# Optimization experiments

Hardware: AMD Instinct MI355X
Metric: run time of the kernel (lower is better)

## Reference

```python
import jax, jax.numpy as jnp
import numpy as np

DIM = 768
HEADS = 12
DIM_HEAD = DIM // HEADS
FACTOR = DIM_HEAD ** (-0.5)
B, T = 4, 2048


def setup_inputs() -> dict:
    key = jax.random.key(0)
    k1, k2, k3 = jax.random.split(key, 3)
    x = jax.random.normal(k1, (B, T, DIM), dtype=jnp.float32)
    # VarianceScaling-like init scale for linear weights
    W_qkv = jax.random.normal(k2, (DIM, 3 * DIM), dtype=jnp.float32) * (DIM ** -0.5)
    W_out = jax.random.normal(k3, (DIM, DIM), dtype=jnp.float32) * (DIM ** -0.5)
    return {"x": x, "W_qkv": W_qkv, "W_out": W_out}


def reference(x, W_qkv, W_out):
    b, t, _ = x.shape
    qkv = x @ W_qkv  # [b, t, 3*dim]
    # einops 'b t (d k h) -> k b h t d' with k=3, h=HEADS: d slowest, k middle, h fastest
    qkv = qkv.reshape(b, t, DIM_HEAD, 3, HEADS)
    qkv = jnp.transpose(qkv, (3, 0, 4, 1, 2))  # [3, b, h, t, d]
    q, k, v = qkv[0], qkv[1], qkv[2]
    # scaled dot-product attention, full [b,h,t,t] scores as in the original
    scores = jnp.einsum('bhid,bhjd->bhij', q, k) * FACTOR
    attn = jax.nn.softmax(scores, axis=-1)
    out = jnp.einsum('bhij,bhjd->bhid', attn, v)  # [b, h, t, d]
    # 'b h t d -> b t (h d)'
    out = jnp.transpose(out, (0, 2, 1, 3)).reshape(b, t, HEADS * DIM_HEAD)
    return out @ W_out
```

## Files before the change

kernel.cpp:

```cpp
#include <hip/hip_runtime.h>
#include <hip/hip_bf16.h>

#define DIM    768
#define HEADS  12
#define DHEAD  64
#define BATCH  4
#define SEQ    2048
#define NROW   (BATCH * SEQ)
#define QKVN   (3 * DIM)
#define FACTOR 0.125f
#define QSCALE 0.18033688011112042f

typedef __attribute__((ext_vector_type(8))) short short8;
typedef __attribute__((ext_vector_type(4))) float floatx4;

__device__ __forceinline__ floatx4 mfma16(short8 a, short8 b, floatx4 c) {
    return __builtin_amdgcn_mfma_f32_16x16x32_bf16(a, b, c, 0, 0, 0);
}

__device__ __forceinline__ void glds16(const void* g, void* l) {
    __builtin_amdgcn_global_load_lds((const __attribute__((address_space(1))) void*)g,
                                     (__attribute__((address_space(3))) void*)l,
                                     16, 0, 0);
}

__device__ __forceinline__ short rne16(float f) {
    unsigned u = __builtin_bit_cast(unsigned, f);
    return (short)((u + 0x7fffu + ((u >> 16) & 1u)) >> 16);
}
__device__ __forceinline__ unsigned pack2(float lo, float hi) {
    unsigned ul = __builtin_bit_cast(unsigned, lo);
    unsigned uh = __builtin_bit_cast(unsigned, hi);
    ul = (ul + 0x7fffu + ((ul >> 16) & 1u)) >> 16;
    uh = (uh + 0x7fffu + ((uh >> 16) & 1u)) & 0xffff0000u;
    return ul | uh;
}
__device__ __forceinline__ unsigned cvtpk(float lo, float hi) {
    unsigned r;
    asm("v_cvt_pk_bf16_f32 %0, %1, %2" : "=v"(r) : "v"(lo), "v"(hi));
    return r;
}

__device__ __forceinline__ int swz8(int row, int col) {
    return (row << 6) + ((((col >> 3) ^ row) & 7) << 3) + (col & 7);
}

__global__ __launch_bounds__(256) void prep(const float* __restrict__ x,
                                            short* __restrict__ xb,
                                            const float* __restrict__ Wqkv,
                                            short* __restrict__ Wqt,
                                            const float* __restrict__ Wout,
                                            short* __restrict__ Wot) {
    __shared__ short T[32][33];
    int blk = blockIdx.x;
    if (blk < 6144) {
        int g = blk * 256 + threadIdx.x;
        float4 v = ((const float4*)x)[g];
        uint2 o;
        o.x = pack2(v.x, v.y);
        o.y = pack2(v.z, v.w);
        ((uint2*)xb)[g] = o;
        return;
    }
    blk -= 6144;
    const float* W;
    short* Wt;
    int N, permute, bx, by;
    if (blk < 1728) { W = Wqkv; Wt = Wqt; N = QKVN; permute = 1; bx = blk % 72; by = blk / 72; }
    else { blk -= 1728; W = Wout; Wt = Wot; N = DIM; permute = 0; bx = blk % 24; by = blk / 24; }

    int n0 = bx * 32, k0 = by * 32;
    int c = threadIdx.x & 31, r0 = threadIdx.x >> 5;
    for (int r = r0; r < 32; r += 8)
        T[r][c] = rne16(W[(size_t)(k0 + r) * N + n0 + c]);
    __syncthreads();
    for (int r = r0; r < 32; r += 8) {
        int n = n0 + r;
        int np = n;
        float scale = 1.0f;
        if (permute) {
            int d = n / 36, rem = n - d * 36;
            int which = rem / 12, h = rem - which * 12;
            np = which * 768 + h * 64 + d;
            if (which == 0) scale = QSCALE;
        }
        float v = __bfloat162float(__hip_bfloat16_raw{(unsigned short)T[c][r]});
        Wt[(size_t)np * DIM + k0 + c] = (scale == 1.0f) ? T[c][r] : rne16(v * scale);
    }
}

__global__ __launch_bounds__(256) void gemm_qkv(const short* __restrict__ A,
                                                const short* __restrict__ Bt,
                                                short* __restrict__ Qo,
                                                short* __restrict__ Ko,
                                                short* __restrict__ Vto) {
    __shared__ short As[128 * 64];
    __shared__ short Bs[128 * 64];
    const int tid = threadIdx.x;
    const int lane = tid & 63, wave = tid >> 6;
    const int l15 = lane & 15, quad = lane >> 4;

    const int flat = blockIdx.x;
    const int xcd = flat & 7;
    const int local = flat >> 3;
    const int mloc = local & 7, nloc = local >> 3;
    const int m0 = (xcd * 8 + mloc) * 128;
    const int n0 = nloc * 128;

    const int wm = (wave >> 1) * 64, wn = (wave & 1) * 64;
    const int r8 = wave * 8 + (lane >> 3);
    const int c8 = lane & 7;
    const int sc = ((c8 ^ (r8 & 7)) << 3);

    const int sn = n0 + wn;
    const int which = sn / 768;
    const bool swapAB = (which != 2);

    floatx4 acc[4][4] = {};
    for (int k0 = 0; k0 < DIM; k0 += 64) {
#pragma unroll
        for (int i = 0; i < 4; ++i) {
            int row = i * 32 + r8;
            glds16(&A[(size_t)(m0 + row) * DIM + k0 + sc], &As[(size_t)(i * 32 + wave * 8) * 64]);
            glds16(&Bt[(size_t)(n0 + row) * DIM + k0 + sc], &Bs[(size_t)(i * 32 + wave * 8) * 64]);
        }
        __syncthreads();
#pragma unroll
        for (int ks = 0; ks < 2; ++ks) {
            short8 a[4], b[4];
#pragma unroll
            for (int mt = 0; mt < 4; ++mt)
                a[mt] = *(const short8*)&As[swz8(wm + mt * 16 + l15, ks * 32 + quad * 8)];
#pragma unroll
            for (int nt = 0; nt < 4; ++nt)
                b[nt] = *(const short8*)&Bs[swz8(wn + nt * 16 + l15, ks * 32 + quad * 8)];
            if (swapAB) {
#pragma unroll
                for (int mt = 0; mt < 4; ++mt)
#pragma unroll
                    for (int nt = 0; nt < 4; ++nt)
                        acc[mt][nt] = mfma16(b[nt], a[mt], acc[mt][nt]);
            } else {
#pragma unroll
                for (int mt = 0; mt < 4; ++mt)
#pragma unroll
                    for (int nt = 0; nt < 4; ++nt)
                        acc[mt][nt] = mfma16(a[mt], b[nt], acc[mt][nt]);
            }
        }
        __syncthreads();
    }

    const int h = (sn - which * 768) >> 6;
    const int bb = (m0 + wm) >> 11;
    const int tbase = (m0 + wm) & 2047;
    const size_t tilebase = ((size_t)(bb * HEADS + h) * 32 + (tbase >> 6)) * 4096;

    if (which != 2) {
        short* dst = (which == 0) ? Qo : Ko;
#pragma unroll
        for (int mt = 0; mt < 4; ++mt)
#pragma unroll
            for (int nt = 0; nt < 4; ++nt) {
                int tl = mt * 16 + l15;
                int d0 = nt * 16 + quad * 4;
                uint2 pk;
                pk.x = pack2(acc[mt][nt][0], acc[mt][nt][1]);
                pk.y = pack2(acc[mt][nt][2], acc[mt][nt][3]);
                *(uint2*)&dst[tilebase + swz8(tl, d0)] = pk;
            }
    } else {
        short* vld = ((wave < 2) ? As : Bs) + (wave & 1) * 4096;
#pragma unroll
        for (int mt = 0; mt < 4; ++mt)
#pragma unroll
            for (int nt = 0; nt < 4; ++nt) {
                int d = nt * 16 + l15;
                int tl = mt * 16 + quad * 4;
                int chunk = (tl >> 3) ^ (d & 7);
                int addr = (d << 6) + (chunk << 3) + (tl & 7);
                uint2 pk;
                pk.x = pack2(acc[mt][nt][0], acc[mt][nt][1]);
                pk.y = pack2(acc[mt][nt][2], acc[mt][nt][3]);
                *(uint2*)&vld[addr] = pk;
            }
    }
    __syncthreads();
    if (which == 2) {
        short* vld = ((wave < 2) ? As : Bs) + (wave & 1) * 4096;
#pragma unroll
        for (int i = 0; i < 8; ++i) {
            int c = (i * 64 + lane) * 8;
            *(uint4*)&Vto[tilebase + c] = *(const uint4*)&vld[c];
        }
    }
}

__global__ __launch_bounds__(256, 3) void attn_mfma(const short* __restrict__ Q,
                                                    const short* __restrict__ K,
                                                    const short* __restrict__ Vt,
                                                    short* __restrict__ O) {
    __shared__ __align__(16) short smem[24576];
    const int tid = threadIdx.x;
    const int lane = tid & 63, wave = tid >> 6;
    const int l15 = lane & 15, quad = lane >> 4;
    const int flat = blockIdx.x;
    const int xcd = flat & 7, li = flat >> 3;
    const int bh = xcd + (li % 6) * 8;
    const int q0 = (li / 6) * 128;
    const size_t base = (size_t)bh * SEQ * DHEAD;
    short* Pp = smem + 16384 + wave * 2048;
    const int lane8 = lane * 8;

    {
        size_t qtb = base + (size_t)(q0 >> 6) * 4096;
#pragma unroll
        for (int c = 0; c < 4; ++c) {
            int i = wave * 4 + c;
            glds16(&Q[qtb + (size_t)i * 512 + lane8], &smem[i * 512]);
        }
    }
    __syncthreads();
    short8 qf[2][2];
#pragma unroll
    for (int mt = 0; mt < 2; ++mt)
#pragma unroll
        for (int ks = 0; ks < 2; ++ks)
            qf[mt][ks] = *(const short8*)&smem[(wave >> 1) * 4096 +
                                               swz8((wave & 1) * 32 + mt * 16 + l15,
                                                    ks * 32 + quad * 8)];
    __syncthreads();

    floatx4 o[4][2] = {};
    float lsum[2] = {0.f, 0.f};

    {
#pragma unroll
        for (int c = 0; c < 2; ++c) {
            int i = wave * 2 + c;
            glds16(&K[base + i * 512 + lane8], &smem[i * 512]);
            glds16(&Vt[base + i * 512 + lane8], &smem[4096 + i * 512]);
        }
    }

    for (int t = 0; t < 32; ++t) {
        __syncthreads();
        short* Ks = smem + (t & 1) * 8192;
        short* Vs = Ks + 4096;
        if (t < 31) {
            size_t ktb = base + (size_t)(t + 1) * 4096;
            short* nb = smem + ((t + 1) & 1) * 8192;
#pragma unroll
            for (int c = 0; c < 2; ++c) {
                int i = wave * 2 + c;
                glds16(&K[ktb + i * 512 + lane8], &nb[i * 512]);
                glds16(&Vt[ktb + i * 512 + lane8], &nb[4096 + i * 512]);
            }
        }

        floatx4 sa[4][2] = {};
        __builtin_amdgcn_s_setprio(1);
#pragma unroll
        for (int ks = 0; ks < 2; ++ks)
#pragma unroll
            for (int kt = 0; kt < 4; ++kt) {
                short8 kf = *(const short8*)&Ks[swz8(kt * 16 + l15, ks * 32 + quad * 8)];
                sa[kt][0] = mfma16(kf, qf[0][ks], sa[kt][0]);
                sa[kt][1] = mfma16(kf, qf[1][ks], sa[kt][1]);
            }
        __builtin_amdgcn_s_setprio(0);

#pragma unroll
        for (int kt = 0; kt < 4; ++kt)
#pragma unroll
            for (int mt = 0; mt < 2; ++mt) {
                float p0 = __builtin_amdgcn_exp2f(sa[kt][mt][0]);
                float p1 = __builtin_amdgcn_exp2f(sa[kt][mt][1]);
                float p2 = __builtin_amdgcn_exp2f(sa[kt][mt][2]);
                float p3 = __builtin_amdgcn_exp2f(sa[kt][mt][3]);
                lsum[mt] += (p0 + p1) + (p2 + p3);
                uint2 pk;
                pk.x = cvtpk(p0, p1);
                pk.y = cvtpk(p2, p3);
                *(uint2*)&Pp[swz8(mt * 16 + l15, kt * 16 + quad * 4)] = pk;
            }

#pragma unroll
        for (int ks = 0; ks < 2; ++ks) {
            short8 pf0 = *(const short8*)&Pp[swz8(l15, ks * 32 + quad * 8)];
            short8 pf1 = *(const short8*)&Pp[swz8(16 + l15, ks * 32 + quad * 8)];
            __builtin_amdgcn_s_setprio(1);
#pragma unroll
            for (int dt = 0; dt < 4; ++dt) {
                short8 vf = *(const short8*)&Vs[swz8(dt * 16 + l15, ks * 32 + quad * 8)];
                o[dt][0] = mfma16(vf, pf0, o[dt][0]);
                o[dt][1] = mfma16(vf, pf1, o[dt][1]);
            }
            __builtin_amdgcn_s_setprio(0);
        }
    }

    float s0 = lsum[0], s1 = lsum[1];
    s0 += __shfl_xor(s0, 16); s0 += __shfl_xor(s0, 32);
    s1 += __shfl_xor(s1, 16); s1 += __shfl_xor(s1, 32);
    float inv0 = 1.f / s0;
    float inv1 = 1.f / s1;

    const int b = bh / HEADS, h = bh - b * HEADS;
#pragma unroll
    for (int mt = 0; mt < 2; ++mt) {
        int tq = q0 + wave * 32 + mt * 16 + l15;
        float iv = mt ? inv1 : inv0;
        size_t rowo = ((size_t)(b * SEQ + tq)) * DIM + h * DHEAD + quad * 4;
#pragma unroll
        for (int dt = 0; dt < 4; ++dt) {
            uint2 pk;
            pk.x = cvtpk(o[dt][mt][0] * iv, o[dt][mt][1] * iv);
            pk.y = cvtpk(o[dt][mt][2] * iv, o[dt][mt][3] * iv);
            *(uint2*)&O[rowo + dt * 16] = pk;
        }
    }
}

__global__ __launch_bounds__(256) void gemm_out(const short* __restrict__ A,
                                                const short* __restrict__ Bt,
                                                float* __restrict__ out) {
    __shared__ short As[128 * 64];
    __shared__ short Bs[128 * 64];
    const int tid = threadIdx.x;
    const int lane = tid & 63, wave = tid >> 6;
    const int l15 = lane & 15, quad = lane >> 4;
    const int m0 = blockIdx.y * 128, n0 = blockIdx.x * 128;
    const int wm = (wave >> 1) * 64, wn = (wave & 1) * 64;
    const int r8 = wave * 8 + (lane >> 3);
    const int sc = (((lane & 7) ^ (r8 & 7)) << 3);

    floatx4 acc[4][4] = {};
    for (int k0 = 0; k0 < DIM; k0 += 64) {
#pragma unroll
        for (int i = 0; i < 4; ++i) {
            int row = i * 32 + r8;
            glds16(&A[(size_t)(m0 + row) * DIM + k0 + sc], &As[(size_t)(i * 32 + wave * 8) * 64]);
            glds16(&Bt[(size_t)(n0 + row) * DIM + k0 + sc], &Bs[(size_t)(i * 32 + wave * 8) * 64]);
        }
        __syncthreads();
#pragma unroll
        for (int ks = 0; ks < 2; ++ks) {
            short8 a[4], b[4];
#pragma unroll
            for (int mt = 0; mt < 4; ++mt)
                a[mt] = *(const short8*)&As[swz8(wm + mt * 16 + l15, ks * 32 + quad * 8)];
#pragma unroll
            for (int nt = 0; nt < 4; ++nt)
                b[nt] = *(const short8*)&Bs[swz8(wn + nt * 16 + l15, ks * 32 + quad * 8)];
#pragma unroll
            for (int mt = 0; mt < 4; ++mt)
#pragma unroll
                for (int nt = 0; nt < 4; ++nt)
                    acc[mt][nt] = mfma16(b[nt], a[mt], acc[mt][nt]);
        }
        __syncthreads();
    }

#pragma unroll
    for (int mt = 0; mt < 4; ++mt)
#pragma unroll
        for (int nt = 0; nt < 4; ++nt) {
            int m = m0 + wm + mt * 16 + l15;
            int n = n0 + wn + nt * 16 + quad * 4;
            *(floatx4*)&out[(size_t)m * DIM + n] = acc[mt][nt];
        }
}

extern "C" void kernel_launch(void* const* d_in, const int* in_sizes, int n_in,
                              void* d_out, int out_size, void* d_ws, size_t ws_size,
                              hipStream_t stream) {
    const float* x    = (const float*)d_in[0];
    const float* Wqkv = (const float*)d_in[1];
    const float* Wout = (const float*)d_in[2];
    float* out = (float*)d_out;

    const size_t NE = (size_t)NROW * DIM;
    short* xb  = (short*)d_ws;
    short* Wqt = xb + NE;
    short* Wot = Wqt + (size_t)QKVN * DIM;
    short* Qw  = Wot + (size_t)DIM * DIM;
    short* Kw  = Qw + NE;
    short* Vtw = Kw + NE;

    prep<<<6144 + 1728 + 576, 256, 0, stream>>>(x, xb, Wqkv, Wqt, Wout, Wot);
    gemm_qkv<<<8 * 8 * 18, 256, 0, stream>>>(xb, Wqt, Qw, Kw, Vtw);
    attn_mfma<<<768, 256, 0, stream>>>(Qw, Kw, Vtw, xb);
    gemm_out<<<dim3(DIM / 128, NROW / 128), 256, 0, stream>>>(xb, Wot, out);
}
```

Before: 213.5 us.

## Split attention query tile across eight waves with one 16-row tile each

The attention kernel now launches 512 threads per block, and each of the eight waves owns 16 query rows instead of 32. The K/V tile loads are spread one chunk per wave and the per-wave P scratch is halved. The goal is more waves in flight per CU to hide LDS and exp latency. In exchange, each K/V fragment read from LDS feeds only one MFMA instead of two, so LDS traffic per MFMA doubles and block barriers now synchronise more waves.

```diff
diff --git a/kernel.cpp b/kernel.cpp
--- a/kernel.cpp
+++ b/kernel.cpp
@@ -196,7 +196,7 @@
     }
 }
 
-__global__ __launch_bounds__(256, 3) void attn_mfma(const short* __restrict__ Q,
+__global__ __launch_bounds__(512, 6) void attn_mfma(const short* __restrict__ Q,
                                                     const short* __restrict__ K,
                                                     const short* __restrict__ Vt,
                                                     short* __restrict__ O) {
@@ -209,39 +209,31 @@
     const int bh = xcd + (li % 6) * 8;
     const int q0 = (li / 6) * 128;
     const size_t base = (size_t)bh * SEQ * DHEAD;
-    short* Pp = smem + 16384 + wave * 2048;
+    short* Pp = smem + 16384 + wave * 1024;
     const int lane8 = lane * 8;
 
     {
         size_t qtb = base + (size_t)(q0 >> 6) * 4096;
 #pragma unroll
-        for (int c = 0; c < 4; ++c) {
-            int i = wave * 4 + c;
-            glds16(&Q[qtb + (size_t)i * 512 + lane8], &smem[i * 512]);
-        }
-    }
-    __syncthreads();
-    short8 qf[2][2];
-#pragma unroll
-    for (int mt = 0; mt < 2; ++mt)
-#pragma unroll
-        for (int ks = 0; ks < 2; ++ks)
-            qf[mt][ks] = *(const short8*)&smem[(wave >> 1) * 4096 +
-                                               swz8((wave & 1) * 32 + mt * 16 + l15,
-                                                    ks * 32 + quad * 8)];
-    __syncthreads();
-
-    floatx4 o[4][2] = {};
-    float lsum[2] = {0.f, 0.f};
-
-    {
-#pragma unroll
         for (int c = 0; c < 2; ++c) {
             int i = wave * 2 + c;
-            glds16(&K[base + i * 512 + lane8], &smem[i * 512]);
-            glds16(&Vt[base + i * 512 + lane8], &smem[4096 + i * 512]);
-        }
-    }
+            glds16(&Q[qtb + (size_t)i * 512 + lane8], &smem[i * 512]);
+        }
+    }
+    __syncthreads();
+    short8 qf[2];
+#pragma unroll
+    for (int ks = 0; ks < 2; ++ks)
+        qf[ks] = *(const short8*)&smem[(wave >> 2) * 4096 +
+                                       swz8((wave & 3) * 16 + l15,
+                                            ks * 32 + quad * 8)];
+    __syncthreads();
+
+    floatx4 o[4] = {};
+    float lsum = 0.f;
+
+    glds16(&K[base + wave * 512 + lane8], &smem[wave * 512]);
+    glds16(&Vt[base + wave * 512 + lane8], &smem[4096 + wave * 512]);
 
     for (int t = 0; t < 32; ++t) {
         __syncthreads();
@@ -250,75 +242,61 @@
         if (t < 31) {
             size_t ktb = base + (size_t)(t + 1) * 4096;
             short* nb = smem + ((t + 1) & 1) * 8192;
-#pragma unroll
-            for (int c = 0; c < 2; ++c) {
-                int i = wave * 2 + c;
-                glds16(&K[ktb + i * 512 + lane8], &nb[i * 512]);
-                glds16(&Vt[ktb + i * 512 + lane8], &nb[4096 + i * 512]);
-            }
-        }
-
-        floatx4 sa[4][2] = {};
+            glds16(&K[ktb + wave * 512 + lane8], &nb[wave * 512]);
+            glds16(&Vt[ktb + wave * 512 + lane8], &nb[4096 + wave * 512]);
+        }
+
+        floatx4 sa[4] = {};
         __builtin_amdgcn_s_setprio(1);
 #pragma unroll
         for (int ks = 0; ks < 2; ++ks)
 #pragma unroll
             for (int kt = 0; kt < 4; ++kt) {
                 short8 kf = *(const short8*)&Ks[swz8(kt * 16 + l15, ks * 32 + quad * 8)];
-                sa[kt][0] = mfma16(kf, qf[0][ks], sa[kt][0]);
-                sa[kt][1] = mfma16(kf, qf[1][ks], sa[kt][1]);
+                sa[kt] = mfma16(kf, qf[ks], sa[kt]);
             }
         __builtin_amdgcn_s_setprio(0);
 
 #pragma unroll
-        for (int kt = 0; kt < 4; ++kt)
-#pragma unroll
-            for (int mt = 0; mt < 2; ++mt) {
-                float p0 = __builtin_amdgcn_exp2f(sa[kt][mt][0]);
-                float p1 = __builtin_amdgcn_exp2f(sa[kt][mt][1]);
-                float p2 = __builtin_amdgcn_exp2f(sa[kt][mt][2]);
-                float p3 = __builtin_amdgcn_exp2f(sa[kt][mt][3]);
-                lsum[mt] += (p0 + p1) + (p2 + p3);
-                uint2 pk;
-                pk.x = cvtpk(p0, p1);
-                pk.y = cvtpk(p2, p3);
-                *(uint2*)&Pp[swz8(mt * 16 + l15, kt * 16 + quad * 4)] = pk;
-            }
+        for (int kt = 0; kt < 4; ++kt) {
+            float p0 = __builtin_amdgcn_exp2f(sa[kt][0]);
+            float p1 = __builtin_amdgcn_exp2f(sa[kt][1]);
+            float p2 = __builtin_amdgcn_exp2f(sa[kt][2]);
+            float p3 = __builtin_amdgcn_exp2f(sa[kt][3]);
+            lsum += (p0 + p1) + (p2 + p3);
+            uint2 pk;
+            pk.x = cvtpk(p0, p1);
+            pk.y = cvtpk(p2, p3);
+            *(uint2*)&Pp[swz8(l15, kt * 16 + quad * 4)] = pk;
+        }
 
 #pragma unroll
         for (int ks = 0; ks < 2; ++ks) {
-            short8 pf0 = *(const short8*)&Pp[swz8(l15, ks * 32 + quad * 8)];
-            short8 pf1 = *(const short8*)&Pp[swz8(16 + l15, ks * 32 + quad * 8)];
+            short8 pf = *(const short8*)&Pp[swz8(l15, ks * 32 + quad * 8)];
             __builtin_amdgcn_s_setprio(1);
 #pragma unroll
             for (int dt = 0; dt < 4; ++dt) {
                 short8 vf = *(const short8*)&Vs[swz8(dt * 16 + l15, ks * 32 + quad * 8)];
-                o[dt][0] = mfma16(vf, pf0, o[dt][0]);
-                o[dt][1] = mfma16(vf, pf1, o[dt][1]);
+                o[dt] = mfma16(vf, pf, o[dt]);
             }
             __builtin_amdgcn_s_setprio(0);
         }
     }
 
-    float s0 = lsum[0], s1 = lsum[1];
-    s0 += __shfl_xor(s0, 16); s0 += __shfl_xor(s0, 32);
-    s1 += __shfl_xor(s1, 16); s1 += __shfl_xor(s1, 32);
-    float inv0 = 1.f / s0;
-    float inv1 = 1.f / s1;
+    float s = lsum;
+    s += __shfl_xor(s, 16);
+    s += __shfl_xor(s, 32);
+    float inv = 1.f / s;
 
     const int b = bh / HEADS, h = bh - b * HEADS;
-#pragma unroll
-    for (int mt = 0; mt < 2; ++mt) {
-        int tq = q0 + wave * 32 + mt * 16 + l15;
-        float iv = mt ? inv1 : inv0;
-        size_t rowo = ((size_t)(b * SEQ + tq)) * DIM + h * DHEAD + quad * 4;
-#pragma unroll
-        for (int dt = 0; dt < 4; ++dt) {
-            uint2 pk;
-            pk.x = cvtpk(o[dt][mt][0] * iv, o[dt][mt][1] * iv);
-            pk.y = cvtpk(o[dt][mt][2] * iv, o[dt][mt][3] * iv);
-            *(uint2*)&O[rowo + dt * 16] = pk;
-        }
+    const int tq = q0 + wave * 16 + l15;
+    size_t rowo = ((size_t)(b * SEQ + tq)) * DIM + h * DHEAD + quad * 4;
+#pragma unroll
+    for (int dt = 0; dt < 4; ++dt) {
+        uint2 pk;
+        pk.x = cvtpk(o[dt][0] * inv, o[dt][1] * inv);
+        pk.y = cvtpk(o[dt][2] * inv, o[dt][3] * inv);
+        *(uint2*)&O[rowo + dt * 16] = pk;
     }
 }
 
@@ -390,6 +368,6 @@
 
     prep<<<6144 + 1728 + 576, 256, 0, stream>>>(x, xb, Wqkv, Wqt, Wout, Wot);
     gemm_qkv<<<8 * 8 * 18, 256, 0, stream>>>(xb, Wqt, Qw, Kw, Vtw);
-    attn_mfma<<<768, 256, 0, stream>>>(Qw, Kw, Vtw, xb);
+    attn_mfma<<<768, 512, 0, stream>>>(Qw, Kw, Vtw, xb);
     gemm_out<<<dim3(DIM / 128, NROW / 128), 256, 0, stream>>>(xb, Wot, out);
 }
```

New measurement: 210.1 us. Within noise of the previous version (-1.6%).
